# Performance work log

Hardware: AMD Instinct MI355X
Metric: run time of the kernel (lower is better)

The kernel has to match this reference:

```python
import jax, jax.numpy as jnp
import numpy as np

B, L, D, A = 64, 512, 512, 512  # batch, seq_len, word_embed_size, alignment_size


def setup_inputs() -> dict:
    key = jax.random.key(0)
    k1, k2, k3 = jax.random.split(key, 3)
    premises = jax.random.normal(k1, (B, L, D), dtype=jnp.float32)
    hypotheses = jax.random.normal(k2, (B, L, D), dtype=jnp.float32)
    W_F = jax.random.uniform(k3, (D, A), dtype=jnp.float32, minval=-1.0, maxval=1.0)
    return {"premises": premises, "hypotheses": hypotheses, "W_F": W_F}


def reference(premises, hypotheses, W_F):
    # tanh-projected cross attention (decomposable-attention align step)
    F_p = jnp.tanh(jnp.einsum('bpd,da->bpa', premises, W_F))    # [B, Lp, A]
    F_h = jnp.tanh(jnp.einsum('bhd,da->bha', hypotheses, W_F))  # [B, Lh, A]
    eijs = jnp.einsum('bpa,bha->bph', F_p, F_h)                 # [B, Lp, Lh] (unscaled)
    attn = jax.nn.softmax(eijs, axis=-1)                        # softmax over hypothesis axis
    betas = jnp.einsum('bph,bhd->bpd', attn, hypotheses)        # [B, Lp, D]
    alphas = jnp.einsum('bph,bpd->bhd', attn, premises)         # [B, Lh, D] (transpose(attn) @ P)
    return betas, alphas
```

## Files before the change

kernel.cpp:

```cpp
#include <hip/hip_runtime.h>
#include <hip/hip_fp16.h>


#define NB 64
#define NL 512
#define ND 512
#define BATCH_ELEMS (512 * 512)
#define TOT_ELEMS   ((size_t)NB * NL * ND)

typedef _Float16 h8 __attribute__((ext_vector_type(8)));
typedef float f4 __attribute__((ext_vector_type(4)));

__device__ __forceinline__ int swz(int row, int chunk) {
    return (row << 5) + ((chunk ^ (((row >> 1) ^ (row >> 4)) & 3)) << 3);
}

__device__ __forceinline__ float fast_tanh(float x) {
    float e = __expf(2.0f * x);
    return 1.0f - 2.0f / (e + 1.0f);
}

template <bool WITH_LO>
__global__ __launch_bounds__(256) void transpose_f16_kernel(
    const float* __restrict__ src, _Float16* __restrict__ dstH,
    _Float16* __restrict__ dstL)
{
    __shared__ float tile[64 * 68];
    const size_t base = (size_t)blockIdx.z * BATCH_ELEMS;
    const int r0 = blockIdx.y * 64, c0 = blockIdx.x * 64;
    const int t = threadIdx.x;
    {
        int r = t >> 2, cq = (t & 3) * 16;
        const float* sp = src + base + (size_t)(r0 + r) * 512 + c0 + cq;
        *(float4*)&tile[r * 68 + cq]      = ((const float4*)sp)[0];
        *(float4*)&tile[r * 68 + cq + 4]  = ((const float4*)sp)[1];
        *(float4*)&tile[r * 68 + cq + 8]  = ((const float4*)sp)[2];
        *(float4*)&tile[r * 68 + cq + 12] = ((const float4*)sp)[3];
    }
    __syncthreads();
    {
        int c = t >> 2, rq = (t & 3) * 16;
        _Float16 hv[16], lv[16];
#pragma unroll
        for (int j = 0; j < 16; ++j) {
            float v = tile[(rq + j) * 68 + c];
            hv[j] = (_Float16)v;
            if (WITH_LO) lv[j] = (_Float16)(v - (float)hv[j]);
        }
        _Float16* dp = dstH + base + (size_t)(c0 + c) * 512 + r0 + rq;
        *(h8*)dp = *(h8*)&hv[0];
        *(h8*)(dp + 8) = *(h8*)&hv[8];
        if (WITH_LO) {
            _Float16* dl = dstL + base + (size_t)(c0 + c) * 512 + r0 + rq;
            *(h8*)dl = *(h8*)&lv[0];
            *(h8*)(dl + 8) = *(h8*)&lv[8];
        }
    }
}

__global__ __launch_bounds__(256) void transpose_hp_kernel(
    const float* __restrict__ H, const float* __restrict__ P,
    _Float16* __restrict__ HT, _Float16* __restrict__ PT)
{
    __shared__ float tile[64 * 68];
    const int z = blockIdx.z;
    const float* src = (z < NB) ? H : P;
    _Float16* dst = (z < NB) ? HT : PT;
    const size_t base = (size_t)(z < NB ? z : z - NB) * BATCH_ELEMS;
    const int r0 = blockIdx.y * 64, c0 = blockIdx.x * 64;
    const int t = threadIdx.x;
    {
        int r = t >> 2, cq = (t & 3) * 16;
        const float* sp = src + base + (size_t)(r0 + r) * 512 + c0 + cq;
        *(float4*)&tile[r * 68 + cq]      = ((const float4*)sp)[0];
        *(float4*)&tile[r * 68 + cq + 4]  = ((const float4*)sp)[1];
        *(float4*)&tile[r * 68 + cq + 8]  = ((const float4*)sp)[2];
        *(float4*)&tile[r * 68 + cq + 12] = ((const float4*)sp)[3];
    }
    __syncthreads();
    {
        int c = t >> 2, rq = (t & 3) * 16;
        _Float16 hv[16];
#pragma unroll
        for (int j = 0; j < 16; ++j) hv[j] = (_Float16)tile[(rq + j) * 68 + c];
        _Float16* dp = dst + base + (size_t)(c0 + c) * 512 + r0 + rq;
        *(h8*)dp = *(h8*)&hv[0];
        *(h8*)(dp + 8) = *(h8*)&hv[8];
    }
}

__global__ __launch_bounds__(256) void proj_tanh_kernel(
    const float* __restrict__ P, const float* __restrict__ H,
    const _Float16* __restrict__ WTH, const _Float16* __restrict__ WTL,
    _Float16* __restrict__ Fout)
{
    __shared__ __align__(16) _Float16 AsH[128 * 32];
    __shared__ __align__(16) _Float16 BsH[128 * 32], BsL[128 * 32];

    const int z = blockIdx.z;
    const float* X = z ? H : P;
    _Float16* F = Fout + (size_t)z * TOT_ELEMS;
    const int r0 = blockIdx.x * 128;
    const int n0 = blockIdx.y * 128;

    const int t = threadIdx.x;
    const int lane = t & 63, w = t >> 6;
    const int q = lane >> 4, c = lane & 15;
    const int wm = w >> 1, wn = w & 1;

    f4 acc[4][4] = {};

    const int ar = t >> 1, akq = (t & 1) << 4;
    const int br = t >> 1, bcp = (t & 1) << 1;

    for (int k0 = 0; k0 < 512; k0 += 32) {
        {
            const float* ap = X + (size_t)(r0 + ar) * 512 + k0 + akq;
            float av[16];
            *(float4*)&av[0]  = ((const float4*)ap)[0];
            *(float4*)&av[4]  = ((const float4*)ap)[1];
            *(float4*)&av[8]  = ((const float4*)ap)[2];
            *(float4*)&av[12] = ((const float4*)ap)[3];
            const int cbase = akq >> 3;
#pragma unroll
            for (int jj = 0; jj < 2; ++jj) {
                h8 hv;
#pragma unroll
                for (int i = 0; i < 8; ++i) hv[i] = (_Float16)av[jj * 8 + i];
                *(h8*)&AsH[swz(ar, cbase + jj)] = hv;
            }
        }
        {
            const _Float16* bh = WTH + (size_t)(n0 + br) * 512 + k0 + bcp * 8;
            const _Float16* bl = WTL + (size_t)(n0 + br) * 512 + k0 + bcp * 8;
            *(h8*)&BsH[swz(br, bcp)]     = ((const h8*)bh)[0];
            *(h8*)&BsH[swz(br, bcp + 1)] = ((const h8*)bh)[1];
            *(h8*)&BsL[swz(br, bcp)]     = ((const h8*)bl)[0];
            *(h8*)&BsL[swz(br, bcp + 1)] = ((const h8*)bl)[1];
        }
        __syncthreads();

        h8 aH[4], bH[4], bL[4];
#pragma unroll
        for (int mi = 0; mi < 4; ++mi) {
            int row = wm * 64 + mi * 16 + c;
            aH[mi] = *(const h8*)&AsH[swz(row, q)];
        }
#pragma unroll
        for (int ni = 0; ni < 4; ++ni) {
            int col = wn * 64 + ni * 16 + c;
            bH[ni] = *(const h8*)&BsH[swz(col, q)];
            bL[ni] = *(const h8*)&BsL[swz(col, q)];
        }
#pragma unroll
        for (int mi = 0; mi < 4; ++mi)
#pragma unroll
            for (int ni = 0; ni < 4; ++ni) {
                acc[mi][ni] = __builtin_amdgcn_mfma_f32_16x16x32_f16(aH[mi], bH[ni], acc[mi][ni], 0, 0, 0);
                acc[mi][ni] = __builtin_amdgcn_mfma_f32_16x16x32_f16(aH[mi], bL[ni], acc[mi][ni], 0, 0, 0);
            }
        __syncthreads();
    }

#pragma unroll
    for (int mi = 0; mi < 4; ++mi)
#pragma unroll
        for (int ni = 0; ni < 4; ++ni) {
            int col = n0 + wn * 64 + ni * 16 + c;
            int rowb = r0 + wm * 64 + mi * 16 + q * 4;
#pragma unroll
            for (int r = 0; r < 4; ++r)
                F[(size_t)(rowb + r) * 512 + col] = (_Float16)fast_tanh(acc[mi][ni][r]);
        }
}

__global__ __launch_bounds__(256) void score_softmax_kernel(
    const _Float16* __restrict__ Fbase, _Float16* __restrict__ attn)
{
    __shared__ __align__(16) _Float16 As[64 * 32];
    __shared__ __align__(16) _Float16 Bs[512 * 32];
    __shared__ float redM[4 * 64], redS[4 * 64];

    const _Float16* Fp = Fbase;
    const _Float16* Fh = Fbase + TOT_ELEMS;
    const int b = blockIdx.y;
    const int p0 = blockIdx.x * 64;
    const size_t fb = (size_t)b * BATCH_ELEMS;

    const int t = threadIdx.x, lane = t & 63, w = t >> 6;
    const int q = lane >> 4, c = lane & 15;

    f4 acc[4][8] = {};

    for (int k0 = 0; k0 < 512; k0 += 32) {
        {
            int row = t >> 2, ch = t & 3;
            *(h8*)&As[swz(row, ch)] =
                *(const h8*)(Fp + fb + (size_t)(p0 + row) * 512 + k0 + ch * 8);
        }
        {
#pragma unroll
            for (int rr = 0; rr < 2; ++rr) {
                int row = t * 2 + rr;
#pragma unroll
                for (int ch = 0; ch < 4; ++ch)
                    *(h8*)&Bs[swz(row, ch)] =
                        *(const h8*)(Fh + fb + (size_t)row * 512 + k0 + ch * 8);
            }
        }
        __syncthreads();

        h8 a[4], bb[8];
#pragma unroll
        for (int mt = 0; mt < 4; ++mt) a[mt] = *(const h8*)&As[swz(mt * 16 + c, q)];
#pragma unroll
        for (int nt = 0; nt < 8; ++nt) bb[nt] = *(const h8*)&Bs[swz(w * 128 + nt * 16 + c, q)];
#pragma unroll
        for (int mt = 0; mt < 4; ++mt)
#pragma unroll
            for (int nt = 0; nt < 8; ++nt)
                acc[mt][nt] = __builtin_amdgcn_mfma_f32_16x16x32_f16(a[mt], bb[nt], acc[mt][nt], 0, 0, 0);
        __syncthreads();
    }

    float rmax[4][4];
#pragma unroll
    for (int mt = 0; mt < 4; ++mt)
#pragma unroll
        for (int r = 0; r < 4; ++r) {
            float m = acc[mt][0][r];
#pragma unroll
            for (int nt = 1; nt < 8; ++nt) m = fmaxf(m, acc[mt][nt][r]);
            rmax[mt][r] = m;
        }
#pragma unroll
    for (int s = 1; s < 16; s <<= 1)
#pragma unroll
        for (int mt = 0; mt < 4; ++mt)
#pragma unroll
            for (int r = 0; r < 4; ++r)
                rmax[mt][r] = fmaxf(rmax[mt][r], __shfl_xor(rmax[mt][r], s, 64));
    if (c == 0)
#pragma unroll
        for (int mt = 0; mt < 4; ++mt)
#pragma unroll
            for (int r = 0; r < 4; ++r)
                redM[w * 64 + mt * 16 + q * 4 + r] = rmax[mt][r];
    __syncthreads();

    float gmax[4][4];
#pragma unroll
    for (int mt = 0; mt < 4; ++mt)
#pragma unroll
        for (int r = 0; r < 4; ++r) {
            int row = mt * 16 + q * 4 + r;
            float m = redM[row];
#pragma unroll
            for (int w4 = 1; w4 < 4; ++w4) m = fmaxf(m, redM[w4 * 64 + row]);
            gmax[mt][r] = m;
        }

    float rsum[4][4] = {};
#pragma unroll
    for (int mt = 0; mt < 4; ++mt)
#pragma unroll
        for (int nt = 0; nt < 8; ++nt)
#pragma unroll
            for (int r = 0; r < 4; ++r) {
                float e = __expf(acc[mt][nt][r] - gmax[mt][r]);
                acc[mt][nt][r] = e;
                rsum[mt][r] += e;
            }
#pragma unroll
    for (int s = 1; s < 16; s <<= 1)
#pragma unroll
        for (int mt = 0; mt < 4; ++mt)
#pragma unroll
            for (int r = 0; r < 4; ++r)
                rsum[mt][r] += __shfl_xor(rsum[mt][r], s, 64);
    if (c == 0)
#pragma unroll
        for (int mt = 0; mt < 4; ++mt)
#pragma unroll
            for (int r = 0; r < 4; ++r)
                redS[w * 64 + mt * 16 + q * 4 + r] = rsum[mt][r];
    __syncthreads();

    float inv[4][4];
#pragma unroll
    for (int mt = 0; mt < 4; ++mt)
#pragma unroll
        for (int r = 0; r < 4; ++r) {
            int row = mt * 16 + q * 4 + r;
            float s = redS[row] + redS[64 + row] + redS[128 + row] + redS[192 + row];
            inv[mt][r] = 1.0f / s;
        }

#pragma unroll
    for (int mt = 0; mt < 4; ++mt)
#pragma unroll
        for (int nt = 0; nt < 8; ++nt) {
            int col = w * 128 + nt * 16 + c;
#pragma unroll
            for (int r = 0; r < 4; ++r) {
                int row = p0 + mt * 16 + q * 4 + r;
                attn[fb + (size_t)row * 512 + col] = (_Float16)(acc[mt][nt][r] * inv[mt][r]);
            }
        }
}

__global__ __launch_bounds__(256) void out_gemm_kernel(
    const _Float16* __restrict__ Amat, const _Float16* __restrict__ HT,
    const _Float16* __restrict__ PT, float* __restrict__ out)
{
    __shared__ __align__(16) _Float16 As[128 * 32];
    __shared__ __align__(16) _Float16 Bs[128 * 32];

    const int zz = blockIdx.z;
    const bool transA = zz >= NB;
    const int b = transA ? zz - NB : zz;
    const _Float16* BT = transA ? PT : HT;
    float* Cout = transA ? out + TOT_ELEMS : out;

    const int bn = blockIdx.x * 128, bm = blockIdx.y * 128;
    const size_t base = (size_t)b * BATCH_ELEMS;

    const int t = threadIdx.x, lane = t & 63, w = t >> 6;
    const int q = lane >> 4, c = lane & 15;
    const int wm = w >> 1, wn = w & 1;

    f4 acc[4][4] = {};

    for (int k0 = 0; k0 < 512; k0 += 32) {
        if (!transA) {
            int row = t >> 1, cp = (t & 1) * 2;
            const _Float16* ap = Amat + base + (size_t)(bm + row) * 512 + k0 + cp * 8;
            *(h8*)&As[swz(row, cp)]     = ((const h8*)ap)[0];
            *(h8*)&As[swz(row, cp + 1)] = ((const h8*)ap)[1];
        } else {
            int kk = t >> 3, m0 = (t & 7) * 16;
            const _Float16* ap = Amat + base + (size_t)(k0 + kk) * 512 + bm + m0;
            h8 x0 = ((const h8*)ap)[0];
            h8 x1 = ((const h8*)ap)[1];
#pragma unroll
            for (int j = 0; j < 8; ++j) {
                As[swz(m0 + j, kk >> 3) + (kk & 7)]     = x0[j];
                As[swz(m0 + 8 + j, kk >> 3) + (kk & 7)] = x1[j];
            }
        }
        {
            int row = t >> 1, cp = (t & 1) * 2;
            const _Float16* bp = BT + base + (size_t)(bn + row) * 512 + k0 + cp * 8;
            *(h8*)&Bs[swz(row, cp)]     = ((const h8*)bp)[0];
            *(h8*)&Bs[swz(row, cp + 1)] = ((const h8*)bp)[1];
        }
        __syncthreads();

        h8 a[4], bb[4];
#pragma unroll
        for (int mi = 0; mi < 4; ++mi) a[mi] = *(const h8*)&As[swz(wm * 64 + mi * 16 + c, q)];
#pragma unroll
        for (int ni = 0; ni < 4; ++ni) bb[ni] = *(const h8*)&Bs[swz(wn * 64 + ni * 16 + c, q)];
#pragma unroll
        for (int mi = 0; mi < 4; ++mi)
#pragma unroll
            for (int ni = 0; ni < 4; ++ni)
                acc[mi][ni] = __builtin_amdgcn_mfma_f32_16x16x32_f16(a[mi], bb[ni], acc[mi][ni], 0, 0, 0);
        __syncthreads();
    }

#pragma unroll
    for (int mi = 0; mi < 4; ++mi)
#pragma unroll
        for (int ni = 0; ni < 4; ++ni) {
            int col = bn + wn * 64 + ni * 16 + c;
            int rowb = bm + wm * 64 + mi * 16 + q * 4;
#pragma unroll
            for (int r = 0; r < 4; ++r)
                Cout[base + (size_t)(rowb + r) * 512 + col] = acc[mi][ni][r];
        }
}

extern "C" void kernel_launch(void* const* d_in, const int* in_sizes, int n_in,
                              void* d_out, int out_size, void* d_ws, size_t ws_size,
                              hipStream_t stream) {
    const float* P = (const float*)d_in[0];
    const float* H = (const float*)d_in[1];
    const float* W = (const float*)d_in[2];
    float* out = (float*)d_out;

    _Float16* ws16 = (_Float16*)d_ws;
    _Float16* F    = ws16;
    _Float16* PT   = ws16;
    _Float16* HT   = ws16 + TOT_ELEMS;
    _Float16* attn = ws16 + 2 * TOT_ELEMS;
    _Float16* WTH  = attn;
    _Float16* WTL  = attn + BATCH_ELEMS;

    transpose_f16_kernel<true><<<dim3(8, 8, 1), 256, 0, stream>>>(W, WTH, WTL);
    proj_tanh_kernel<<<dim3(256, 4, 2), 256, 0, stream>>>(P, H, WTH, WTL, F);
    score_softmax_kernel<<<dim3(8, NB), 256, 0, stream>>>(F, attn);
    transpose_hp_kernel<<<dim3(8, 8, 2 * NB), 256, 0, stream>>>(H, P, HT, PT);
    out_gemm_kernel<<<dim3(4, 4, 2 * NB), 256, 0, stream>>>(attn, HT, PT, out);
}
```

Measured before the change: 481.2 us.

## Double-buffer LDS tiles with register prefetch in all three GEMM kernels

```diff
diff --git a/kernel.cpp b/kernel.cpp
--- a/kernel.cpp
+++ b/kernel.cpp
@@ -94,8 +94,8 @@
     const _Float16* __restrict__ WTH, const _Float16* __restrict__ WTL,
     _Float16* __restrict__ Fout)
 {
-    __shared__ __align__(16) _Float16 AsH[128 * 32];
-    __shared__ __align__(16) _Float16 BsH[128 * 32], BsL[128 * 32];
+    __shared__ __align__(16) _Float16 AsH[2][128 * 32];
+    __shared__ __align__(16) _Float16 BsH[2][128 * 32], BsL[2][128 * 32];
 
     const int z = blockIdx.z;
     const float* X = z ? H : P;
@@ -113,44 +113,61 @@
     const int ar = t >> 1, akq = (t & 1) << 4;
     const int br = t >> 1, bcp = (t & 1) << 1;
 
+    const float* apg = X + (size_t)(r0 + ar) * 512 + akq;
+    const _Float16* bhg = WTH + (size_t)(n0 + br) * 512 + bcp * 8;
+    const _Float16* blg = WTL + (size_t)(n0 + br) * 512 + bcp * 8;
+
+    float av[16];
+    h8 bh0, bh1, bl0, bl1;
+
+    auto LOAD = [&](int k0) {
+        *(float4*)&av[0]  = ((const float4*)(apg + k0))[0];
+        *(float4*)&av[4]  = ((const float4*)(apg + k0))[1];
+        *(float4*)&av[8]  = ((const float4*)(apg + k0))[2];
+        *(float4*)&av[12] = ((const float4*)(apg + k0))[3];
+        bh0 = ((const h8*)(bhg + k0))[0];
+        bh1 = ((const h8*)(bhg + k0))[1];
+        bl0 = ((const h8*)(blg + k0))[0];
+        bl1 = ((const h8*)(blg + k0))[1];
+    };
+    auto STAGE = [&](int pp) {
+        _Float16* asd = &AsH[pp][0];
+        _Float16* bhd = &BsH[pp][0];
+        _Float16* bld = &BsL[pp][0];
+        const int cbase = akq >> 3;
+#pragma unroll
+        for (int jj = 0; jj < 2; ++jj) {
+            h8 hv;
+#pragma unroll
+            for (int i = 0; i < 8; ++i) hv[i] = (_Float16)av[jj * 8 + i];
+            *(h8*)&asd[swz(ar, cbase + jj)] = hv;
+        }
+        *(h8*)&bhd[swz(br, bcp)]     = bh0;
+        *(h8*)&bhd[swz(br, bcp + 1)] = bh1;
+        *(h8*)&bld[swz(br, bcp)]     = bl0;
+        *(h8*)&bld[swz(br, bcp + 1)] = bl1;
+    };
+
+    LOAD(0);
+    STAGE(0);
+
+    int pp = 0;
     for (int k0 = 0; k0 < 512; k0 += 32) {
-        {
-            const float* ap = X + (size_t)(r0 + ar) * 512 + k0 + akq;
-            float av[16];
-            *(float4*)&av[0]  = ((const float4*)ap)[0];
-            *(float4*)&av[4]  = ((const float4*)ap)[1];
-            *(float4*)&av[8]  = ((const float4*)ap)[2];
-            *(float4*)&av[12] = ((const float4*)ap)[3];
-            const int cbase = akq >> 3;
-#pragma unroll
-            for (int jj = 0; jj < 2; ++jj) {
-                h8 hv;
-#pragma unroll
-                for (int i = 0; i < 8; ++i) hv[i] = (_Float16)av[jj * 8 + i];
-                *(h8*)&AsH[swz(ar, cbase + jj)] = hv;
-            }
-        }
-        {
-            const _Float16* bh = WTH + (size_t)(n0 + br) * 512 + k0 + bcp * 8;
-            const _Float16* bl = WTL + (size_t)(n0 + br) * 512 + k0 + bcp * 8;
-            *(h8*)&BsH[swz(br, bcp)]     = ((const h8*)bh)[0];
-            *(h8*)&BsH[swz(br, bcp + 1)] = ((const h8*)bh)[1];
-            *(h8*)&BsL[swz(br, bcp)]     = ((const h8*)bl)[0];
-            *(h8*)&BsL[swz(br, bcp + 1)] = ((const h8*)bl)[1];
-        }
         __syncthreads();
-
+        const bool more = (k0 + 32) < 512;
+        if (more) LOAD(k0 + 32);
+
+        const _Float16* ash = &AsH[pp][0];
+        const _Float16* bhs = &BsH[pp][0];
+        const _Float16* bls = &BsL[pp][0];
         h8 aH[4], bH[4], bL[4];
 #pragma unroll
-        for (int mi = 0; mi < 4; ++mi) {
-            int row = wm * 64 + mi * 16 + c;
-            aH[mi] = *(const h8*)&AsH[swz(row, q)];
-        }
+        for (int mi = 0; mi < 4; ++mi)
+            aH[mi] = *(const h8*)&ash[swz(wm * 64 + mi * 16 + c, q)];
 #pragma unroll
         for (int ni = 0; ni < 4; ++ni) {
-            int col = wn * 64 + ni * 16 + c;
-            bH[ni] = *(const h8*)&BsH[swz(col, q)];
-            bL[ni] = *(const h8*)&BsL[swz(col, q)];
+            bH[ni] = *(const h8*)&bhs[swz(wn * 64 + ni * 16 + c, q)];
+            bL[ni] = *(const h8*)&bls[swz(wn * 64 + ni * 16 + c, q)];
         }
 #pragma unroll
         for (int mi = 0; mi < 4; ++mi)
@@ -159,7 +176,8 @@
                 acc[mi][ni] = __builtin_amdgcn_mfma_f32_16x16x32_f16(aH[mi], bH[ni], acc[mi][ni], 0, 0, 0);
                 acc[mi][ni] = __builtin_amdgcn_mfma_f32_16x16x32_f16(aH[mi], bL[ni], acc[mi][ni], 0, 0, 0);
             }
-        __syncthreads();
+        if (more) STAGE(pp ^ 1);
+        pp ^= 1;
     }
 
 #pragma unroll
@@ -177,8 +195,8 @@
 __global__ __launch_bounds__(256) void score_softmax_kernel(
     const _Float16* __restrict__ Fbase, _Float16* __restrict__ attn)
 {
-    __shared__ __align__(16) _Float16 As[64 * 32];
-    __shared__ __align__(16) _Float16 Bs[512 * 32];
+    __shared__ __align__(16) _Float16 As[2][64 * 32];
+    __shared__ __align__(16) _Float16 Bs[2][512 * 32];
     __shared__ float redM[4 * 64], redS[4 * 64];
 
     const _Float16* Fp = Fbase;
@@ -192,35 +210,50 @@
 
     f4 acc[4][8] = {};
 
+    const int arow = t >> 2, ach = t & 3;
+    const _Float16* apg = Fp + fb + (size_t)(p0 + arow) * 512 + ach * 8;
+    const _Float16* bpg = Fh + fb + (size_t)(t * 2) * 512;
+
+    h8 areg, breg[2][4];
+
+    auto LOAD = [&](int k0) {
+        areg = *(const h8*)(apg + k0);
+#pragma unroll
+        for (int rr = 0; rr < 2; ++rr)
+#pragma unroll
+            for (int ch = 0; ch < 4; ++ch)
+                breg[rr][ch] = *(const h8*)(bpg + (size_t)rr * 512 + k0 + ch * 8);
+    };
+    auto STAGE = [&](int pp) {
+        *(h8*)&As[pp][swz(arow, ach)] = areg;
+#pragma unroll
+        for (int rr = 0; rr < 2; ++rr)
+#pragma unroll
+            for (int ch = 0; ch < 4; ++ch)
+                *(h8*)&Bs[pp][swz(t * 2 + rr, ch)] = breg[rr][ch];
+    };
+
+    LOAD(0);
+    STAGE(0);
+
+    int pp = 0;
     for (int k0 = 0; k0 < 512; k0 += 32) {
-        {
-            int row = t >> 2, ch = t & 3;
-            *(h8*)&As[swz(row, ch)] =
-                *(const h8*)(Fp + fb + (size_t)(p0 + row) * 512 + k0 + ch * 8);
-        }
-        {
-#pragma unroll
-            for (int rr = 0; rr < 2; ++rr) {
-                int row = t * 2 + rr;
-#pragma unroll
-                for (int ch = 0; ch < 4; ++ch)
-                    *(h8*)&Bs[swz(row, ch)] =
-                        *(const h8*)(Fh + fb + (size_t)row * 512 + k0 + ch * 8);
-            }
-        }
         __syncthreads();
+        const bool more = (k0 + 32) < 512;
+        if (more) LOAD(k0 + 32);
 
         h8 a[4], bb[8];
 #pragma unroll
-        for (int mt = 0; mt < 4; ++mt) a[mt] = *(const h8*)&As[swz(mt * 16 + c, q)];
-#pragma unroll
-        for (int nt = 0; nt < 8; ++nt) bb[nt] = *(const h8*)&Bs[swz(w * 128 + nt * 16 + c, q)];
+        for (int mt = 0; mt < 4; ++mt) a[mt] = *(const h8*)&As[pp][swz(mt * 16 + c, q)];
+#pragma unroll
+        for (int nt = 0; nt < 8; ++nt) bb[nt] = *(const h8*)&Bs[pp][swz(w * 128 + nt * 16 + c, q)];
 #pragma unroll
         for (int mt = 0; mt < 4; ++mt)
 #pragma unroll
             for (int nt = 0; nt < 8; ++nt)
                 acc[mt][nt] = __builtin_amdgcn_mfma_f32_16x16x32_f16(a[mt], bb[nt], acc[mt][nt], 0, 0, 0);
-        __syncthreads();
+        if (more) STAGE(pp ^ 1);
+        pp ^= 1;
     }
 
     float rmax[4][4];
@@ -313,8 +346,8 @@
     const _Float16* __restrict__ Amat, const _Float16* __restrict__ HT,
     const _Float16* __restrict__ PT, float* __restrict__ out)
 {
-    __shared__ __align__(16) _Float16 As[128 * 32];
-    __shared__ __align__(16) _Float16 Bs[128 * 32];
+    __shared__ __align__(16) _Float16 As[2][128 * 32];
+    __shared__ __align__(16) _Float16 Bs[2][128 * 32];
 
     const int zz = blockIdx.z;
     const bool transA = zz >= NB;
@@ -331,42 +364,61 @@
 
     f4 acc[4][4] = {};
 
+    const int row2 = t >> 1, cp2 = (t & 1) * 2;
+    const int kk = t >> 3, m0 = (t & 7) * 16;
+    const _Float16* apg_d = Amat + base + (size_t)(bm + row2) * 512 + cp2 * 8;
+    const _Float16* apg_t = Amat + base + (size_t)kk * 512 + bm + m0;
+    const _Float16* bpg   = BT + base + (size_t)(bn + row2) * 512 + cp2 * 8;
+
+    h8 a0, a1, b0, b1;
+
+    auto LOAD = [&](int k0) {
+        if (!transA) {
+            a0 = ((const h8*)(apg_d + k0))[0];
+            a1 = ((const h8*)(apg_d + k0))[1];
+        } else {
+            a0 = ((const h8*)(apg_t + (size_t)k0 * 512))[0];
+            a1 = ((const h8*)(apg_t + (size_t)k0 * 512))[1];
+        }
+        b0 = ((const h8*)(bpg + k0))[0];
+        b1 = ((const h8*)(bpg + k0))[1];
+    };
+    auto STAGE = [&](int pp) {
+        if (!transA) {
+            *(h8*)&As[pp][swz(row2, cp2)]     = a0;
+            *(h8*)&As[pp][swz(row2, cp2 + 1)] = a1;
+        } else {
+#pragma unroll
+            for (int j = 0; j < 8; ++j) {
+                As[pp][swz(m0 + j, kk >> 3) + (kk & 7)]     = a0[j];
+                As[pp][swz(m0 + 8 + j, kk >> 3) + (kk & 7)] = a1[j];
+            }
+        }
+        *(h8*)&Bs[pp][swz(row2, cp2)]     = b0;
+        *(h8*)&Bs[pp][swz(row2, cp2 + 1)] = b1;
+    };
+
+    LOAD(0);
+    STAGE(0);
+
+    int pp = 0;
     for (int k0 = 0; k0 < 512; k0 += 32) {
-        if (!transA) {
-            int row = t >> 1, cp = (t & 1) * 2;
-            const _Float16* ap = Amat + base + (size_t)(bm + row) * 512 + k0 + cp * 8;
-            *(h8*)&As[swz(row, cp)]     = ((const h8*)ap)[0];
-            *(h8*)&As[swz(row, cp + 1)] = ((const h8*)ap)[1];
-        } else {
-            int kk = t >> 3, m0 = (t & 7) * 16;
-            const _Float16* ap = Amat + base + (size_t)(k0 + kk) * 512 + bm + m0;
-            h8 x0 = ((const h8*)ap)[0];
-            h8 x1 = ((const h8*)ap)[1];
-#pragma unroll
-            for (int j = 0; j < 8; ++j) {
-                As[swz(m0 + j, kk >> 3) + (kk & 7)]     = x0[j];
-                As[swz(m0 + 8 + j, kk >> 3) + (kk & 7)] = x1[j];
-            }
-        }
-        {
-            int row = t >> 1, cp = (t & 1) * 2;
-            const _Float16* bp = BT + base + (size_t)(bn + row) * 512 + k0 + cp * 8;
-            *(h8*)&Bs[swz(row, cp)]     = ((const h8*)bp)[0];
-            *(h8*)&Bs[swz(row, cp + 1)] = ((const h8*)bp)[1];
-        }
         __syncthreads();
+        const bool more = (k0 + 32) < 512;
+        if (more) LOAD(k0 + 32);
 
         h8 a[4], bb[4];
 #pragma unroll
-        for (int mi = 0; mi < 4; ++mi) a[mi] = *(const h8*)&As[swz(wm * 64 + mi * 16 + c, q)];
-#pragma unroll
-        for (int ni = 0; ni < 4; ++ni) bb[ni] = *(const h8*)&Bs[swz(wn * 64 + ni * 16 + c, q)];
+        for (int mi = 0; mi < 4; ++mi) a[mi] = *(const h8*)&As[pp][swz(wm * 64 + mi * 16 + c, q)];
+#pragma unroll
+        for (int ni = 0; ni < 4; ++ni) bb[ni] = *(const h8*)&Bs[pp][swz(wn * 64 + ni * 16 + c, q)];
 #pragma unroll
         for (int mi = 0; mi < 4; ++mi)
 #pragma unroll
             for (int ni = 0; ni < 4; ++ni)
                 acc[mi][ni] = __builtin_amdgcn_mfma_f32_16x16x32_f16(a[mi], bb[ni], acc[mi][ni], 0, 0, 0);
-        __syncthreads();
+        if (more) STAGE(pp ^ 1);
+        pp ^= 1;
     }
 
 #pragma unroll
```

After: 473.4 us. No clear change (-1.6%).
